# Kernel tuning notes

Measured on AMD Instinct MI355X. Metric: run time of the kernel, lower is better.

The kernel has to match this reference:

```python
import jax, jax.numpy as jnp
import numpy as np

B, T, A, P = 128, 128, 16, 4
D, H, Q, QI, V = 256, 512, 128, 512, 64
NUM_TRICKS = 13
SIGNAL_PHASE = 1
# static phase routing: contiguous blocks of T/P positions per phase (phase_mask buffer)
PHASE_ID = (np.arange(T) * P // T).astype(np.int32)
_DECAY = 0.6
_nt_left = NUM_TRICKS - np.arange(NUM_TRICKS, dtype=np.float32)
P_SIGNAL = ((1.0 - _DECAY) / (1.0 - _DECAY ** _nt_left)).astype(np.float32)


def setup_inputs() -> dict:
    key = jax.random.key(0)
    ks = jax.random.split(key, 12)
    a = jax.random.randint(ks[0], (B, T, A, 3), 0, V, dtype=jnp.int32)
    pad = (jax.random.uniform(ks[1], (B, T, A)) < 0.3) & (jnp.arange(A) >= 1)
    valid_actions = jnp.where(pad[..., None], -1, a)
    phase = jnp.broadcast_to(jnp.asarray(PHASE_ID), (B, T)).astype(jnp.int32)
    trick = jax.random.randint(ks[2], (B, T), 0, NUM_TRICKS, dtype=jnp.int32)
    backbone_embed = jax.random.normal(ks[3], (B, T, QI), jnp.float32)
    s = lambda k, shape, fan: jax.random.normal(k, shape, jnp.float32) / np.float32(np.sqrt(fan))
    return dict(
        backbone_embed=backbone_embed, valid_actions=valid_actions, phase=phase, trick=trick,
        emb0=s(ks[4], (V, D), D), emb1=s(ks[5], (V, D), D), emb2=s(ks[6], (V, D), D),
        ln_g=jnp.ones((D,), jnp.float32), ln_b=jnp.zeros((D,), jnp.float32),
        kW1=s(ks[7], (P, D, H), D), kb1=jnp.zeros((P, H), jnp.float32),
        kW2=s(ks[8], (P, H, H), H), kb2=jnp.zeros((P, H), jnp.float32),
        kW3=s(ks[9], (P, H, Q), H), kb3=jnp.zeros((P, Q), jnp.float32),
        qW=s(ks[10], (P, QI, Q), QI), qb=jnp.zeros((P, Q), jnp.float32),
    )


def _forward(backbone_embed, valid_actions, phase, trick,
             emb0, emb1, emb2, ln_g, ln_b,
             kW1, kb1, kW2, kb2, kW3, kb3, qW, qb):
    pid = PHASE_ID  # static (T,) routing -> gather per-position phase params (same math as mask gather/scatter)
    idx = jnp.clip(valid_actions, 0, V - 1)
    x = emb0[idx[..., 0]] + emb1[idx[..., 1]] + emb2[idx[..., 2]]  # (B,T,A,D) action embed
    mu = jnp.mean(x, -1, keepdims=True)
    var = jnp.var(x, -1, keepdims=True)
    x = (x - mu) * jax.lax.rsqrt(var + 1e-5) * ln_g + ln_b  # key LayerNorm
    # phase-branched key MLP (BranchedFF over MLP)
    h = jax.nn.relu(jnp.einsum('btad,tdh->btah', x, kW1[pid]) + kb1[pid][None, :, None, :])
    h = jax.nn.relu(jnp.einsum('btah,thg->btag', h, kW2[pid]) + kb2[pid][None, :, None, :])
    keyv = jnp.einsum('btah,thq->btaq', h, kW3[pid]) + kb3[pid][None, :, None, :]  # (B,T,A,Q)
    # phase-branched query Linear (BranchedFF over Linear)
    query = jnp.einsum('btd,tdq->btq', backbone_embed, qW[pid]) + qb[pid][None]  # (B,T,Q)
    attn = jnp.einsum('btq,btaq->bta', query, keyv) / np.float32(np.sqrt(Q))
    invalid = valid_actions[..., 0] == -1
    attn = jnp.where(invalid, -jnp.inf, attn)
    # no-signal log-weight
    n_valid = jnp.sum(~invalid, -1).astype(attn.dtype)  # (B,T)
    p_s = jnp.asarray(P_SIGNAL)[trick]
    wgt = jnp.log(jnp.maximum((1.0 - p_s) / p_s * (n_valid - 1.0), 1e-5))
    wgt = jnp.where(n_valid == 1.0, 0.0, wgt)
    attn = attn.at[..., 0].add(jnp.where(phase == SIGNAL_PHASE, wgt, 0.0))
    return jax.nn.log_softmax(attn, axis=-1)


def reference(backbone_embed, valid_actions, phase, trick,
              emb0, emb1, emb2, ln_g, ln_b,
              kW1, kb1, kW2, kb2, kW3, kb3, qW, qb):
    return _forward(backbone_embed, valid_actions, phase, trick,
                    emb0, emb1, emb2, ln_g, ln_b,
                    kW1, kb1, kW2, kb2, kW3, kb3, qW, qb)
```

## Files before the change

kernel.cpp:

```cpp
#include <hip/hip_runtime.h>
#include <hip/hip_bf16.h>
#include <cmath>

constexpr int Bc = 128, Tc = 128, Ac = 16;
constexpr int Dc = 256, Hc = 512, Qc = 128, QIc = 512, Vc = 64, NTk = 13;
constexpr float NEG_BIG = -1e30f;
constexpr float ACT_SCALE = 16.f;
constexpr float ACC_SCALE = 1.f / 256.f;
constexpr float ACC_TO_ACT = 1.f / 16.f;

typedef unsigned int uint;
typedef uint uint2v __attribute__((ext_vector_type(2)));
typedef float f32x4 __attribute__((ext_vector_type(4)));

#define MFMA16F8(a, b, c) __builtin_amdgcn_mfma_f32_16x16x32_fp8_fp8(a, b, c, 0, 0, 0)

__device__ __forceinline__ long long u2ll(uint2v v) {
  union { uint2v u; long long l; } x;
  x.u = v;
  return x.l;
}
__device__ __forceinline__ unsigned short f2bfu(float f) {
  __hip_bfloat16 h = __float2bfloat16(f);
  return *(unsigned short*)&h;
}
__device__ __forceinline__ float bf2f(short s) {
  return __uint_as_float(((unsigned)(unsigned short)s) << 16);
}
__device__ __forceinline__ uint pack4_fp8(float a, float b, float c, float d) {
  uint v = 0;
  v = __builtin_amdgcn_cvt_pk_fp8_f32(a, b, v, 0);
  v = __builtin_amdgcn_cvt_pk_fp8_f32(c, d, v, 1);
  return v;
}

__global__ void transform_all(const float* __restrict__ kW1, const float* __restrict__ kW2,
                              const float* __restrict__ kW3, const float* __restrict__ qW,
                              uint2v* __restrict__ kW1f, uint2v* __restrict__ kW2f,
                              uint2v* __restrict__ kW3f, uint2v* __restrict__ qWf) {
  int gid = blockIdx.x * 256 + threadIdx.x;
  const float* W;
  uint2v* dst;
  int NT, KC, N, local;
  if (gid < 65536) {
    W = kW1; dst = kW1f; NT = 32; KC = 8; N = 512; local = gid;
  } else if (gid < 196608) {
    W = kW2; dst = kW2f; NT = 32; KC = 16; N = 512; local = gid - 65536;
  } else if (gid < 229376) {
    W = kW3; dst = kW3f; NT = 8; KC = 16; N = 128; local = gid - 196608;
  } else {
    W = qW; dst = qWf; NT = 8; KC = 16; N = 128; local = gid - 229376;
  }
  int lane = local & 63;
  int frag = local >> 6;
  int kc = frag % KC;
  int rest = frag / KC;
  int nt = rest % NT;
  int p = rest / NT;
  int K = KC * 32;
  int n = nt * 16 + (lane & 15);
  int k0 = kc * 32 + (lane >> 4) * 8;
  const float* src = W + ((size_t)p * K + k0) * N + n;
  float f[8];
#pragma unroll
  for (int j = 0; j < 8; ++j) f[j] = src[(size_t)j * N] * ACT_SCALE;
  uint2v v;
  v.x = pack4_fp8(f[0], f[1], f[2], f[3]);
  v.y = pack4_fp8(f[4], f[5], f[6], f[7]);
  dst[local] = v;
}

template <int KC, int WT, int AT, bool RELU, int OUTMODE, int SIN, int SOUT>
__device__ __forceinline__ void layer16(
    const char* __restrict__ aB, void* __restrict__ o0,
    const uint2v* __restrict__ Wf, const float* __restrict__ bias,
    int wt0, int lane) {
  const int c = lane & 15, q = lane >> 4;
  const char* ap = aB + c * SIN + q * 8;

  f32x4 acc[WT][AT];
#pragma unroll
  for (int wt = 0; wt < WT; ++wt)
#pragma unroll
    for (int at = 0; at < AT; ++at)
#pragma unroll
      for (int r = 0; r < 4; ++r) acc[wt][at][r] = 0.f;

#pragma unroll 1
  for (int kc = 0; kc < KC; ++kc) {
    uint2v bf[AT];
#pragma unroll
    for (int at = 0; at < AT; ++at)
      bf[at] = *(const uint2v*)(ap + at * 16 * SIN + kc * 32);
#pragma unroll
    for (int wt = 0; wt < WT; ++wt) {
      const uint2v* wk = Wf + ((size_t)(wt0 + wt) * KC + kc) * 64;
      uint2v wv = wk[lane];
      long long ww = u2ll(wv);
#pragma unroll
      for (int at = 0; at < AT; ++at)
        acc[wt][at] = MFMA16F8(ww, u2ll(bf[at]), acc[wt][at]);
    }
  }

#pragma unroll
  for (int wt = 0; wt < WT; ++wt) {
    const int nb = (wt0 + wt) * 16 + 4 * q;
    float4 bv = *(const float4*)(bias + nb);
#pragma unroll
    for (int at = 0; at < AT; ++at) {
      const int row = at * 16 + c;
      if (OUTMODE == 0) {
        float s0 = fmaf(acc[wt][at][0], ACC_TO_ACT, bv.x * ACT_SCALE);
        float s1 = fmaf(acc[wt][at][1], ACC_TO_ACT, bv.y * ACT_SCALE);
        float s2 = fmaf(acc[wt][at][2], ACC_TO_ACT, bv.z * ACT_SCALE);
        float s3 = fmaf(acc[wt][at][3], ACC_TO_ACT, bv.w * ACT_SCALE);
        if (RELU) {
          s0 = fmaxf(s0, 0.f); s1 = fmaxf(s1, 0.f);
          s2 = fmaxf(s2, 0.f); s3 = fmaxf(s3, 0.f);
        }
        *(uint*)((char*)o0 + row * SOUT + nb) = pack4_fp8(s0, s1, s2, s3);
      } else if (OUTMODE == 1) {
        float s0 = fmaf(acc[wt][at][0], ACC_SCALE, bv.x);
        float s1 = fmaf(acc[wt][at][1], ACC_SCALE, bv.y);
        float s2 = fmaf(acc[wt][at][2], ACC_SCALE, bv.z);
        float s3 = fmaf(acc[wt][at][3], ACC_SCALE, bv.w);
        uint2v u;
        u.x = ((uint)f2bfu(s1) << 16) | f2bfu(s0);
        u.y = ((uint)f2bfu(s3) << 16) | f2bfu(s2);
        *(uint2v*)((short*)o0 + row * SOUT + nb) = u;
      } else {
        if (c < 4) {
          float4 st;
          st.x = fmaf(acc[wt][at][0], ACC_SCALE, bv.x);
          st.y = fmaf(acc[wt][at][1], ACC_SCALE, bv.y);
          st.z = fmaf(acc[wt][at][2], ACC_SCALE, bv.z);
          st.w = fmaf(acc[wt][at][3], ACC_SCALE, bv.w);
          *(float4*)((float*)o0 + c * SOUT + nb) = st;
        }
      }
    }
  }
}

constexpr int SX = 280;
constexpr int SH = 536;
constexpr int SKV = 136;
constexpr int SQY = 132;

__global__ __launch_bounds__(1024, 8) void policy_main(
    const float* __restrict__ be, const int* __restrict__ va,
    const int* __restrict__ phase, const int* __restrict__ trick,
    const float* __restrict__ emb0, const float* __restrict__ emb1,
    const float* __restrict__ emb2, const float* __restrict__ ln_g,
    const float* __restrict__ ln_b,
    const float* __restrict__ kb1, const float* __restrict__ kb2,
    const float* __restrict__ kb3, const float* __restrict__ qb,
    const uint2v* __restrict__ kW1f, const uint2v* __restrict__ kW2f,
    const uint2v* __restrict__ kW3f, const uint2v* __restrict__ qWf,
    float* __restrict__ out) {
  __shared__ __align__(16) char bufA[64 * SH];
  __shared__ __align__(16) char bufB[64 * SH];
  __shared__ __align__(16) char beAb[16 * SH];
  __shared__ __align__(16) float QYs[4 * SQY];
  __shared__ float attn_s[64];
  __shared__ int inval_s[64];
  __shared__ int ph_s[4], tr_s[4];

  char* Xs = bufA;
  char* H2 = bufA;
  char* H1 = bufB;
  short* KV = (short*)bufB;

  const int tid = threadIdx.x;
  const int w = tid >> 6, lane = tid & 63;
  const int p = blockIdx.x & 3;
  const int g = blockIdx.x >> 2;
  const int b = g >> 3;
  const int t0 = p * 32 + (g & 7) * 4;
  const int bt0 = b * Tc + t0;

  if (tid < 64) {
    inval_s[tid] = (va[((size_t)bt0 * Ac + tid) * 3] == -1);
  } else if (tid < 68) {
    ph_s[tid - 64] = phase[bt0 + tid - 64];
  } else if (tid < 72) {
    tr_s[tid - 68] = trick[bt0 + tid - 68];
  }
  if (tid < 256) {
    int tok = tid >> 6, d0 = (tid & 63) * 8;
    const float* bp = be + ((size_t)bt0 + tok) * QIc + d0;
    uint2v v8;
    v8.x = pack4_fp8(bp[0] * ACT_SCALE, bp[1] * ACT_SCALE, bp[2] * ACT_SCALE, bp[3] * ACT_SCALE);
    v8.y = pack4_fp8(bp[4] * ACT_SCALE, bp[5] * ACT_SCALE, bp[6] * ACT_SCALE, bp[7] * ACT_SCALE);
    *(uint2v*)(beAb + tok * SH + d0) = v8;
  }
  {
    const int r = tid >> 4, part = tid & 15, d0 = part * 16;
    const int* vp = va + ((size_t)bt0 * Ac + r) * 3;
    int i0 = min(max(vp[0], 0), Vc - 1);
    int i1 = min(max(vp[1], 0), Vc - 1);
    int i2 = min(max(vp[2], 0), Vc - 1);
    const float4* e0 = (const float4*)(emb0 + i0 * Dc + d0);
    const float4* e1 = (const float4*)(emb1 + i1 * Dc + d0);
    const float4* e2 = (const float4*)(emb2 + i2 * Dc + d0);
    float xv[16];
    float sum = 0.f, ss = 0.f;
#pragma unroll
    for (int j = 0; j < 4; ++j) {
      float4 v0 = e0[j], v1 = e1[j], v2 = e2[j];
      float4 v;
      v.x = v0.x + v1.x + v2.x; v.y = v0.y + v1.y + v2.y;
      v.z = v0.z + v1.z + v2.z; v.w = v0.w + v1.w + v2.w;
      xv[j * 4 + 0] = v.x; xv[j * 4 + 1] = v.y; xv[j * 4 + 2] = v.z; xv[j * 4 + 3] = v.w;
      sum += v.x + v.y + v.z + v.w;
      ss += v.x * v.x + v.y * v.y + v.z * v.z + v.w * v.w;
    }
    sum += __shfl_xor(sum, 1); sum += __shfl_xor(sum, 2);
    sum += __shfl_xor(sum, 4); sum += __shfl_xor(sum, 8);
    ss += __shfl_xor(ss, 1);   ss += __shfl_xor(ss, 2);
    ss += __shfl_xor(ss, 4);   ss += __shfl_xor(ss, 8);
    const float mu = sum / (float)Dc;
    const float rstd = rsqrtf(ss / (float)Dc - mu * mu + 1e-5f);
    float y[16];
#pragma unroll
    for (int j = 0; j < 16; ++j) {
      int d = d0 + j;
      y[j] = ((xv[j] - mu) * rstd * ln_g[d] + ln_b[d]) * ACT_SCALE;
    }
    uint2v v8;
    v8.x = pack4_fp8(y[0], y[1], y[2], y[3]);
    v8.y = pack4_fp8(y[4], y[5], y[6], y[7]);
    *(uint2v*)(Xs + r * SX + d0) = v8;
    v8.x = pack4_fp8(y[8], y[9], y[10], y[11]);
    v8.y = pack4_fp8(y[12], y[13], y[14], y[15]);
    *(uint2v*)(Xs + r * SX + d0 + 8) = v8;
  }
  __syncthreads();

  layer16<8, 2, 4, true, 0, SX, SH>(Xs, H1, kW1f + (size_t)p * 32 * 8 * 64,
                                    kb1 + p * Hc, w * 2, lane);
  __syncthreads();

  layer16<16, 2, 4, true, 0, SH, SH>(H1, H2, kW2f + (size_t)p * 32 * 16 * 64,
                                     kb2 + p * Hc, w * 2, lane);
  __syncthreads();

  if (w < 8) {
    layer16<16, 1, 4, false, 1, SH, SKV>(H2, KV, kW3f + (size_t)p * 8 * 16 * 64,
                                         kb3 + p * Qc, w, lane);
  } else {
    layer16<16, 1, 1, false, 2, SH, SQY>(beAb, QYs, qWf + (size_t)p * 8 * 16 * 64,
                                         qb + p * Qc, w - 8, lane);
  }
  __syncthreads();

  {
    const int r = tid >> 4, part = tid & 15, tok = r >> 4;
    const short* kp = KV + r * SKV + part * 8;
    const float* qp = QYs + tok * SQY + part * 8;
    float s = 0.f;
#pragma unroll
    for (int j = 0; j < 8; ++j) s += bf2f(kp[j]) * qp[j];
    s += __shfl_xor(s, 1); s += __shfl_xor(s, 2);
    s += __shfl_xor(s, 4); s += __shfl_xor(s, 8);
    if (part == 0) attn_s[r] = s * 0.08838834764831845f;
  }
  __syncthreads();

  if (tid < 4) {
    const int tok = tid;
    const int bt = bt0 + tok;
    float av[Ac];
    int nv = 0;
#pragma unroll
    for (int a = 0; a < Ac; ++a) {
      int iv = inval_s[tok * Ac + a];
      nv += iv ? 0 : 1;
      av[a] = iv ? NEG_BIG : attn_s[tok * Ac + a];
    }
    if (ph_s[tok] == 1) {
      const int nt = NTk - tr_s[tok];
      float dp = 1.f;
      for (int i = 0; i < nt; ++i) dp *= 0.6f;
      const float ps = 0.4f / (1.f - dp);
      float wgt = (nv == 1) ? 0.f : logf(fmaxf((1.f - ps) / ps * ((float)nv - 1.f), 1e-5f));
      av[0] += wgt;
    }
    float m = NEG_BIG;
#pragma unroll
    for (int a = 0; a < Ac; ++a) m = fmaxf(m, av[a]);
    float s = 0.f;
#pragma unroll
    for (int a = 0; a < Ac; ++a) s += expf(av[a] - m);
    const float lse = logf(s) + m;
#pragma unroll
    for (int a = 0; a < Ac; ++a)
      out[bt * Ac + a] = inval_s[tok * Ac + a] ? NEG_BIG : (av[a] - lse);
  }
}

extern "C" void kernel_launch(void* const* d_in, const int* in_sizes, int n_in,
                              void* d_out, int out_size, void* d_ws, size_t ws_size,
                              hipStream_t stream) {
  const float* be   = (const float*)d_in[0];
  const int*   va   = (const int*)d_in[1];
  const int*   ph   = (const int*)d_in[2];
  const int*   tr   = (const int*)d_in[3];
  const float* emb0 = (const float*)d_in[4];
  const float* emb1 = (const float*)d_in[5];
  const float* emb2 = (const float*)d_in[6];
  const float* lng  = (const float*)d_in[7];
  const float* lnb  = (const float*)d_in[8];
  const float* kW1  = (const float*)d_in[9];
  const float* kb1  = (const float*)d_in[10];
  const float* kW2  = (const float*)d_in[11];
  const float* kb2  = (const float*)d_in[12];
  const float* kW3  = (const float*)d_in[13];
  const float* kb3  = (const float*)d_in[14];
  const float* qW   = (const float*)d_in[15];
  const float* qb   = (const float*)d_in[16];
  float* out = (float*)d_out;

  uint2v* kW1f = (uint2v*)d_ws;
  uint2v* kW2f = kW1f + 65536;
  uint2v* kW3f = kW2f + 131072;
  uint2v* qWf  = kW3f + 32768;

  transform_all<<<262144 / 256, 256, 0, stream>>>(kW1, kW2, kW3, qW, kW1f, kW2f, kW3f, qWf);

  policy_main<<<4096, 1024, 0, stream>>>(be, va, ph, tr, emb0, emb1, emb2, lng, lnb,
                                         kb1, kb2, kb3, qb, kW1f, kW2f, kW3f, qWf, out);
}
```

Baseline: 337.6 us.

## Pair K-chunks into 16-byte fragments for wider LDS and weight loads

Measured after the change: 393.7 us. 16.6% more time.

```diff
diff --git a/kernel.cpp b/kernel.cpp
--- a/kernel.cpp
+++ b/kernel.cpp
@@ -11,13 +11,14 @@
 
 typedef unsigned int uint;
 typedef uint uint2v __attribute__((ext_vector_type(2)));
+typedef uint uint4v __attribute__((ext_vector_type(4)));
 typedef float f32x4 __attribute__((ext_vector_type(4)));
 
 #define MFMA16F8(a, b, c) __builtin_amdgcn_mfma_f32_16x16x32_fp8_fp8(a, b, c, 0, 0, 0)
 
-__device__ __forceinline__ long long u2ll(uint2v v) {
-  union { uint2v u; long long l; } x;
-  x.u = v;
+__device__ __forceinline__ long long mk_ll(uint lo, uint hi) {
+  union { uint u[2]; long long l; } x;
+  x.u[0] = lo; x.u[1] = hi;
   return x.l;
 }
 __device__ __forceinline__ unsigned short f2bfu(float f) {
@@ -36,47 +37,53 @@
 
 __global__ void transform_all(const float* __restrict__ kW1, const float* __restrict__ kW2,
                               const float* __restrict__ kW3, const float* __restrict__ qW,
-                              uint2v* __restrict__ kW1f, uint2v* __restrict__ kW2f,
-                              uint2v* __restrict__ kW3f, uint2v* __restrict__ qWf) {
+                              uint4v* __restrict__ kW1f, uint4v* __restrict__ kW2f,
+                              uint4v* __restrict__ kW3f, uint4v* __restrict__ qWf) {
   int gid = blockIdx.x * 256 + threadIdx.x;
   const float* W;
-  uint2v* dst;
-  int NT, KC, N, local;
-  if (gid < 65536) {
-    W = kW1; dst = kW1f; NT = 32; KC = 8; N = 512; local = gid;
-  } else if (gid < 196608) {
-    W = kW2; dst = kW2f; NT = 32; KC = 16; N = 512; local = gid - 65536;
-  } else if (gid < 229376) {
-    W = kW3; dst = kW3f; NT = 8; KC = 16; N = 128; local = gid - 196608;
+  uint4v* dst;
+  int NT, KCP, N, local;
+  if (gid < 32768) {
+    W = kW1; dst = kW1f; NT = 32; KCP = 4; N = 512; local = gid;
+  } else if (gid < 98304) {
+    W = kW2; dst = kW2f; NT = 32; KCP = 8; N = 512; local = gid - 32768;
+  } else if (gid < 114688) {
+    W = kW3; dst = kW3f; NT = 8; KCP = 8; N = 128; local = gid - 98304;
   } else {
-    W = qW; dst = qWf; NT = 8; KC = 16; N = 128; local = gid - 229376;
+    W = qW; dst = qWf; NT = 8; KCP = 8; N = 128; local = gid - 114688;
   }
   int lane = local & 63;
   int frag = local >> 6;
-  int kc = frag % KC;
-  int rest = frag / KC;
+  int kcp = frag % KCP;
+  int rest = frag / KCP;
   int nt = rest % NT;
   int p = rest / NT;
-  int K = KC * 32;
+  int K = KCP * 64;
   int n = nt * 16 + (lane & 15);
-  int k0 = kc * 32 + (lane >> 4) * 8;
+  int k0 = kcp * 64 + (lane >> 4) * 8;
   const float* src = W + ((size_t)p * K + k0) * N + n;
-  float f[8];
-#pragma unroll
-  for (int j = 0; j < 8; ++j) f[j] = src[(size_t)j * N] * ACT_SCALE;
-  uint2v v;
+  float f[8], g[8];
+#pragma unroll
+  for (int j = 0; j < 8; ++j) {
+    f[j] = src[(size_t)j * N] * ACT_SCALE;
+    g[j] = src[(size_t)(j + 32) * N] * ACT_SCALE;
+  }
+  uint4v v;
   v.x = pack4_fp8(f[0], f[1], f[2], f[3]);
   v.y = pack4_fp8(f[4], f[5], f[6], f[7]);
+  v.z = pack4_fp8(g[0], g[1], g[2], g[3]);
+  v.w = pack4_fp8(g[4], g[5], g[6], g[7]);
   dst[local] = v;
 }
 
-template <int KC, int WT, int AT, bool RELU, int OUTMODE, int SIN, int SOUT>
+template <int KC, int WT, int AT, bool RELU, int OUTMODE, int SROW, int QB, int OA, int OB>
 __device__ __forceinline__ void layer16(
     const char* __restrict__ aB, void* __restrict__ o0,
-    const uint2v* __restrict__ Wf, const float* __restrict__ bias,
+    const uint4v* __restrict__ Wf, const float* __restrict__ bias,
     int wt0, int lane) {
   const int c = lane & 15, q = lane >> 4;
-  const char* ap = aB + c * SIN + q * 8;
+  const char* ap = aB + c * SROW + q * QB;
+  constexpr int KCP = KC / 2;
 
   f32x4 acc[WT][AT];
 #pragma unroll
@@ -87,19 +94,22 @@
       for (int r = 0; r < 4; ++r) acc[wt][at][r] = 0.f;
 
 #pragma unroll 1
-  for (int kc = 0; kc < KC; ++kc) {
-    uint2v bf[AT];
+  for (int kcp = 0; kcp < KCP; ++kcp) {
+    uint4v af[AT];
 #pragma unroll
     for (int at = 0; at < AT; ++at)
-      bf[at] = *(const uint2v*)(ap + at * 16 * SIN + kc * 32);
+      af[at] = *(const uint4v*)(ap + at * 16 * SROW + kcp * 16);
 #pragma unroll
     for (int wt = 0; wt < WT; ++wt) {
-      const uint2v* wk = Wf + ((size_t)(wt0 + wt) * KC + kc) * 64;
-      uint2v wv = wk[lane];
-      long long ww = u2ll(wv);
-#pragma unroll
-      for (int at = 0; at < AT; ++at)
-        acc[wt][at] = MFMA16F8(ww, u2ll(bf[at]), acc[wt][at]);
+      const uint4v* wk = Wf + ((size_t)(wt0 + wt) * KCP + kcp) * 64;
+      uint4v wv = wk[lane];
+      long long wlo = mk_ll(wv.x, wv.y);
+      long long whi = mk_ll(wv.z, wv.w);
+#pragma unroll
+      for (int at = 0; at < AT; ++at) {
+        acc[wt][at] = MFMA16F8(wlo, mk_ll(af[at].x, af[at].y), acc[wt][at]);
+        acc[wt][at] = MFMA16F8(whi, mk_ll(af[at].z, af[at].w), acc[wt][at]);
+      }
     }
   }
 
@@ -119,7 +129,8 @@
           s0 = fmaxf(s0, 0.f); s1 = fmaxf(s1, 0.f);
           s2 = fmaxf(s2, 0.f); s3 = fmaxf(s3, 0.f);
         }
-        *(uint*)((char*)o0 + row * SOUT + nb) = pack4_fp8(s0, s1, s2, s3);
+        const int kco = nb >> 5, qo = (nb & 31) >> 3, jo = nb & 7;
+        *(uint*)((char*)o0 + row * OA + qo * OB + kco * 8 + jo) = pack4_fp8(s0, s1, s2, s3);
       } else if (OUTMODE == 1) {
         float s0 = fmaf(acc[wt][at][0], ACC_SCALE, bv.x);
         float s1 = fmaf(acc[wt][at][1], ACC_SCALE, bv.y);
@@ -128,7 +139,7 @@
         uint2v u;
         u.x = ((uint)f2bfu(s1) << 16) | f2bfu(s0);
         u.y = ((uint)f2bfu(s3) << 16) | f2bfu(s2);
-        *(uint2v*)((short*)o0 + row * SOUT + nb) = u;
+        *(uint2v*)((short*)o0 + row * OA + nb) = u;
       } else {
         if (c < 4) {
           float4 st;
@@ -136,15 +147,17 @@
           st.y = fmaf(acc[wt][at][1], ACC_SCALE, bv.y);
           st.z = fmaf(acc[wt][at][2], ACC_SCALE, bv.z);
           st.w = fmaf(acc[wt][at][3], ACC_SCALE, bv.w);
-          *(float4*)((float*)o0 + c * SOUT + nb) = st;
+          *(float4*)((float*)o0 + c * OA + nb) = st;
         }
       }
     }
   }
 }
 
-constexpr int SX = 280;
-constexpr int SH = 536;
+constexpr int QB_X = 64;
+constexpr int SROW_X = 272;
+constexpr int QB_H = 128;
+constexpr int SROW_H = 560;
 constexpr int SKV = 136;
 constexpr int SQY = 132;
 
@@ -156,21 +169,21 @@
     const float* __restrict__ ln_b,
     const float* __restrict__ kb1, const float* __restrict__ kb2,
     const float* __restrict__ kb3, const float* __restrict__ qb,
-    const uint2v* __restrict__ kW1f, const uint2v* __restrict__ kW2f,
-    const uint2v* __restrict__ kW3f, const uint2v* __restrict__ qWf,
+    const uint4v* __restrict__ kW1f, const uint4v* __restrict__ kW2f,
+    const uint4v* __restrict__ kW3f, const uint4v* __restrict__ qWf,
     float* __restrict__ out) {
-  __shared__ __align__(16) char bufA[64 * SH];
-  __shared__ __align__(16) char bufB[64 * SH];
-  __shared__ __align__(16) char beAb[16 * SH];
-  __shared__ __align__(16) float QYs[4 * SQY];
+  __shared__ __align__(16) char bufA[64 * SROW_H];
+  __shared__ __align__(16) char bufB[64 * SROW_H];
+  __shared__ __align__(16) char beAb[16 * SROW_H];
   __shared__ float attn_s[64];
-  __shared__ int inval_s[64];
+  __shared__ char inval_s[64];
   __shared__ int ph_s[4], tr_s[4];
 
   char* Xs = bufA;
   char* H2 = bufA;
   char* H1 = bufB;
   short* KV = (short*)bufB;
+  float* QYs = (float*)(bufB + 64 * SKV * 2);
 
   const int tid = threadIdx.x;
   const int w = tid >> 6, lane = tid & 63;
@@ -188,12 +201,13 @@
     tr_s[tid - 68] = trick[bt0 + tid - 68];
   }
   if (tid < 256) {
-    int tok = tid >> 6, d0 = (tid & 63) * 8;
-    const float* bp = be + ((size_t)bt0 + tok) * QIc + d0;
+    int tok = tid >> 6, i = tid & 63;
+    int kc = i >> 2, qq = i & 3;
+    const float* bp = be + ((size_t)bt0 + tok) * QIc + kc * 32 + qq * 8;
     uint2v v8;
     v8.x = pack4_fp8(bp[0] * ACT_SCALE, bp[1] * ACT_SCALE, bp[2] * ACT_SCALE, bp[3] * ACT_SCALE);
     v8.y = pack4_fp8(bp[4] * ACT_SCALE, bp[5] * ACT_SCALE, bp[6] * ACT_SCALE, bp[7] * ACT_SCALE);
-    *(uint2v*)(beAb + tok * SH + d0) = v8;
+    *(uint2v*)(beAb + tok * SROW_H + qq * QB_H + kc * 8) = v8;
   }
   {
     const int r = tid >> 4, part = tid & 15, d0 = part * 16;
@@ -228,30 +242,31 @@
       int d = d0 + j;
       y[j] = ((xv[j] - mu) * rstd * ln_g[d] + ln_b[d]) * ACT_SCALE;
     }
+    const int kc = part >> 1, q1 = (part & 1) * 2;
     uint2v v8;
     v8.x = pack4_fp8(y[0], y[1], y[2], y[3]);
     v8.y = pack4_fp8(y[4], y[5], y[6], y[7]);
-    *(uint2v*)(Xs + r * SX + d0) = v8;
+    *(uint2v*)(Xs + r * SROW_X + q1 * QB_X + kc * 8) = v8;
     v8.x = pack4_fp8(y[8], y[9], y[10], y[11]);
     v8.y = pack4_fp8(y[12], y[13], y[14], y[15]);
-    *(uint2v*)(Xs + r * SX + d0 + 8) = v8;
-  }
-  __syncthreads();
-
-  layer16<8, 2, 4, true, 0, SX, SH>(Xs, H1, kW1f + (size_t)p * 32 * 8 * 64,
-                                    kb1 + p * Hc, w * 2, lane);
-  __syncthreads();
-
-  layer16<16, 2, 4, true, 0, SH, SH>(H1, H2, kW2f + (size_t)p * 32 * 16 * 64,
-                                     kb2 + p * Hc, w * 2, lane);
+    *(uint2v*)(Xs + r * SROW_X + (q1 + 1) * QB_X + kc * 8) = v8;
+  }
+  __syncthreads();
+
+  layer16<8, 2, 4, true, 0, SROW_X, QB_X, SROW_H, QB_H>(
+      Xs, H1, kW1f + (size_t)p * 8192, kb1 + p * Hc, w * 2, lane);
+  __syncthreads();
+
+  layer16<16, 2, 4, true, 0, SROW_H, QB_H, SROW_H, QB_H>(
+      H1, H2, kW2f + (size_t)p * 16384, kb2 + p * Hc, w * 2, lane);
   __syncthreads();
 
   if (w < 8) {
-    layer16<16, 1, 4, false, 1, SH, SKV>(H2, KV, kW3f + (size_t)p * 8 * 16 * 64,
-                                         kb3 + p * Qc, w, lane);
+    layer16<16, 1, 4, false, 1, SROW_H, QB_H, SKV, 0>(
+        H2, KV, kW3f + (size_t)p * 4096, kb3 + p * Qc, w, lane);
   } else {
-    layer16<16, 1, 1, false, 2, SH, SQY>(beAb, QYs, qWf + (size_t)p * 8 * 16 * 64,
-                                         qb + p * Qc, w - 8, lane);
+    layer16<16, 1, 1, false, 2, SROW_H, QB_H, SQY, 0>(
+        beAb, QYs, qWf + (size_t)p * 4096, qb + p * Qc, w - 8, lane);
   }
   __syncthreads();
 
@@ -322,12 +337,12 @@
   const float* qb   = (const float*)d_in[16];
   float* out = (float*)d_out;
 
-  uint2v* kW1f = (uint2v*)d_ws;
-  uint2v* kW2f = kW1f + 65536;
-  uint2v* kW3f = kW2f + 131072;
-  uint2v* qWf  = kW3f + 32768;
-
-  transform_all<<<262144 / 256, 256, 0, stream>>>(kW1, kW2, kW3, qW, kW1f, kW2f, kW3f, qWf);
+  uint4v* kW1f = (uint4v*)d_ws;
+  uint4v* kW2f = kW1f + 32768;
+  uint4v* kW3f = kW2f + 65536;
+  uint4v* qWf  = kW3f + 16384;
+
+  transform_all<<<131072 / 256, 256, 0, stream>>>(kW1, kW2, kW3, qW, kW1f, kW2f, kW3f, qWf);
 
   policy_main<<<4096, 1024, 0, stream>>>(be, va, ph, tr, emb0, emb1, emb2, lng, lnb,
                                          kb1, kb2, kb3, qb, kW1f, kW2f, kW3f, qWf, out);
```
